# Optimization experiments

Hardware: AMD Instinct MI355X
Metric: run time of the kernel (lower is better)

The kernel has to match this reference:

```python
import jax, jax.numpy as jnp
import numpy as np

G, IN_DIM, OUT_DIM = 100000, 256, 128
B, N = 4096, 8192
ALPHA = 0.2          # LeakyReLU negative slope
NEG_INF = -9e15      # same masking constant as the torch module
EPS = 1e-12          # F.normalize eps


def setup_inputs() -> dict:
    key = jax.random.key(0)
    k1, k2, k3, k4, k5, k6, k7 = jax.random.split(key, 7)
    global_feature = jax.random.normal(k1, (G, IN_DIM), dtype=jnp.float32)
    nodes = jax.random.randint(k2, (B,), 0, G, dtype=jnp.int32)
    unique_nodes = jax.random.randint(k3, (N,), 0, G, dtype=jnp.int32)
    mask = jax.random.randint(k4, (B, N), 0, 2, dtype=jnp.int32)
    # ensure every row has at least one neighbor (original always includes self)
    mask = mask.at[:, 0].set(1)
    # xavier_uniform with gain=1.414
    gain = 1.414
    lim_W = gain * np.sqrt(6.0 / (IN_DIM + OUT_DIM))
    W = jax.random.uniform(k5, (IN_DIM, OUT_DIM), jnp.float32, -lim_W, lim_W)
    lim_a = gain * np.sqrt(6.0 / (2 * OUT_DIM + 1))
    a1 = jax.random.uniform(k6, (OUT_DIM,), jnp.float32, -lim_a, lim_a)
    a2 = jax.random.uniform(k7, (OUT_DIM,), jnp.float32, -lim_a, lim_a)
    return {"global_feature": global_feature, "nodes": nodes,
            "unique_nodes": unique_nodes, "mask": mask,
            "W": W, "a1": a1, "a2": a2}


def reference(global_feature, nodes, unique_nodes, mask, W, a1, a2):
    # project gathered features: [B,F], [N,F]
    h_nodes = global_feature[nodes] @ W
    h_neigh = global_feature[unique_nodes] @ W
    # additive attention scores; equivalent to cat([h_i,h_j]) @ a
    e = h_nodes @ a1[:, None] + (h_neigh @ a2)[None, :]   # [B,N]
    e = jnp.where(e >= 0, e, ALPHA * e)                    # leaky relu
    e = jnp.where(mask > 0, e, NEG_INF)
    attention = jax.nn.softmax(e, axis=1)                  # [B,N]
    out = attention @ h_neigh                              # [B,F]
    norm = jnp.linalg.norm(out, axis=1, keepdims=True)
    out = out / jnp.maximum(norm, EPS)                     # F.normalize p=2
    return out
```

## Files before the change

### kernel.cpp

```cpp
#include <hip/hip_runtime.h>
#include <hip/hip_bf16.h>

#define IN_DIM  256
#define OUT_DIM 128
#define B_ROWS  4096
#define N_COLS  8192
#define ALPHA   0.2f
#define NS      4

typedef unsigned short u16;
typedef unsigned int   u32;
typedef __attribute__((ext_vector_type(8))) short short8;
typedef __attribute__((ext_vector_type(4))) float floatx4;

__device__ __forceinline__ float bf2f(u16 v){ return __uint_as_float(((u32)v) << 16); }
__device__ __forceinline__ float bflo(u32 v){ return __uint_as_float(v << 16); }
__device__ __forceinline__ float bfhi(u32 v){ return __uint_as_float(v & 0xffff0000u); }
__device__ __forceinline__ u16 f2bf(float f){
    u32 u = __float_as_uint(f);
    u += 0x7fffu + ((u >> 16) & 1u);
    return (u16)(u >> 16);
}
__device__ __forceinline__ u32 pack_bf16(float a, float b){
    __hip_bfloat162 h = __float22bfloat162_rn(make_float2(a, b));
    return *reinterpret_cast<u32*>(&h);
}

__device__ __forceinline__ int detect_bf16_wave(const u32* __restrict__ g){
    int lane = threadIdx.x & 63;
    uint4 u = ((const uint4*)g)[lane];
#define CHK(x) ((((x) >> 7) & 0xFF) >= 110 && (((x) >> 7) & 0xFF) <= 140)
    unsigned long long c0 = __ballot(CHK(u.x)), c1 = __ballot(CHK(u.y));
    unsigned long long c2 = __ballot(CHK(u.z)), c3 = __ballot(CHK(u.w));
#undef CHK
    int votes = __popcll(c0) + __popcll(c1) + __popcll(c2) + __popcll(c3);
    return votes >= 128;
}

__global__ __launch_bounds__(128) void k_prep(const void* __restrict__ gf,
                                              const void* __restrict__ W, const void* __restrict__ a1,
                                              const void* __restrict__ a2,
                                              u16* __restrict__ WB, float* __restrict__ Wa1,
                                              float* __restrict__ a2f){
    const int isbf = detect_bf16_wave((const u32*)gf);
    const int c  = threadIdx.x;
    const int kb = blockIdx.x;
    float a1c = isbf ? bf2f(((const u16*)a1)[c]) : ((const float*)a1)[c];
    float w[8]; short8 v;
#pragma unroll
    for (int j = 0; j < 8; j++){
        w[j] = isbf ? bf2f(((const u16*)W)[(kb*8 + j) * OUT_DIM + c])
                    : ((const float*)W)[(kb*8 + j) * OUT_DIM + c];
        v[j] = (short)f2bf(w[j]);
    }
    ((short8*)WB)[kb * OUT_DIM + c] = v;

    __shared__ float red[2][8];
    int lane = c & 63, wv = c >> 6;
#pragma unroll
    for (int j = 0; j < 8; j++){
        float p = w[j] * a1c;
        p += __shfl_xor(p, 1);  p += __shfl_xor(p, 2);  p += __shfl_xor(p, 4);
        p += __shfl_xor(p, 8);  p += __shfl_xor(p, 16); p += __shfl_xor(p, 32);
        if (lane == 0) red[wv][j] = p;
    }
    __syncthreads();
    if (c < 8) Wa1[kb*8 + c] = red[0][c] + red[1][c];
    if (kb == 0) a2f[c] = isbf ? bf2f(((const u16*)a2)[c]) : ((const float*)a2)[c];
}

__global__ __launch_bounds__(256) void k_hneigh(const void* __restrict__ gf, const int* __restrict__ uniq,
                                                const u16* __restrict__ WB, const float* __restrict__ a2f,
                                                u16* __restrict__ hB, float2* __restrict__ esg2){
    const int n0   = blockIdx.x * 16;
    const int t    = threadIdx.x;
    const int lane = t & 63;
    const int wv   = t >> 6;
    const int q    = lane >> 4;
    const int m    = lane & 15;
    const int isbf = detect_bf16_wave((const u32*)gf);
    const int jb0  = wv * 2;

    const size_t row = (size_t)uniq[n0 + m];
    const short8* wb8 = (const short8*)WB;

    floatx4 acc0 = {0.f,0.f,0.f,0.f};
    floatx4 acc1 = {0.f,0.f,0.f,0.f};

#pragma unroll
    for (int ks = 0; ks < IN_DIM/32; ks++){
        short8 afrag;
        if (isbf){
            afrag = *(const short8*)((const u16*)gf + row * IN_DIM + ks*32 + q*8);
        } else {
            const float* gp = (const float*)gf + row * IN_DIM + ks*32 + q*8;
            float4 f0 = *(const float4*)gp;
            float4 f1 = *(const float4*)(gp + 4);
            afrag[0] = (short)f2bf(f0.x); afrag[1] = (short)f2bf(f0.y);
            afrag[2] = (short)f2bf(f0.z); afrag[3] = (short)f2bf(f0.w);
            afrag[4] = (short)f2bf(f1.x); afrag[5] = (short)f2bf(f1.y);
            afrag[6] = (short)f2bf(f1.z); afrag[7] = (short)f2bf(f1.w);
        }
        const int kb = ks*4 + q;
        short8 b0 = wb8[kb * OUT_DIM + jb0*16 + m];
        short8 b1 = wb8[kb * OUT_DIM + (jb0+1)*16 + m];
        acc0 = __builtin_amdgcn_mfma_f32_16x16x32_bf16(afrag, b0, acc0, 0, 0, 0);
        acc1 = __builtin_amdgcn_mfma_f32_16x16x32_bf16(afrag, b1, acc1, 0, 0, 0);
    }

    {
        uint2 v0, v1;
        v0.x = (u32)f2bf(acc0[0]) | ((u32)f2bf(acc0[1]) << 16);
        v0.y = (u32)f2bf(acc0[2]) | ((u32)f2bf(acc0[3]) << 16);
        v1.x = (u32)f2bf(acc1[0]) | ((u32)f2bf(acc1[1]) << 16);
        v1.y = (u32)f2bf(acc1[2]) | ((u32)f2bf(acc1[3]) << 16);
        u16* base = hB + (size_t)(n0/8 + (q>>1)) * 1024 + (q&1)*4;
        *(uint2*)(base + (jb0*16 + m) * 8)     = v0;
        *(uint2*)(base + ((jb0+1)*16 + m) * 8) = v1;
    }

    __shared__ float sred[4][16];
    float a2c0 = a2f[jb0*16 + m], a2c1 = a2f[(jb0+1)*16 + m];
#pragma unroll
    for (int reg = 0; reg < 4; reg++){
        float pr = acc0[reg]*a2c0 + acc1[reg]*a2c1;
        pr += __shfl_xor(pr, 1); pr += __shfl_xor(pr, 2);
        pr += __shfl_xor(pr, 4); pr += __shfl_xor(pr, 8);
        if (m == 0) sred[wv][q*4 + reg] = pr;
    }
    __syncthreads();
    if (t < 16){
        float s = sred[0][t] + sred[1][t] + sred[2][t] + sred[3][t];
        s = fminf(fmaxf(s, -40.f), 40.f);
        esg2[n0 + t] = make_float2(__expf(s), __expf(ALPHA * s));
    }
}

__global__ __launch_bounds__(256) void k_esn(const void* __restrict__ gf, const int* __restrict__ nodes,
                                             const float* __restrict__ Wa1, float2* __restrict__ esn2){
    int lane = threadIdx.x & 63, wv = threadIdx.x >> 6;
    int b = blockIdx.x * 4 + wv;
    const int isbf = detect_bf16_wave((const u32*)gf);
    float4 wa = ((const float4*)Wa1)[lane];
    float x0, x1, x2, x3;
    if (isbf){
        uint2 gg = ((const uint2*)((const u16*)gf + (size_t)nodes[b] * IN_DIM))[lane];
        x0 = bflo(gg.x); x1 = bfhi(gg.x); x2 = bflo(gg.y); x3 = bfhi(gg.y);
    } else {
        float4 gg = ((const float4*)((const float*)gf + (size_t)nodes[b] * IN_DIM))[lane];
        x0 = gg.x; x1 = gg.y; x2 = gg.z; x3 = gg.w;
    }
    float s = x0*wa.x + x1*wa.y + x2*wa.z + x3*wa.w;
    s += __shfl_xor(s, 1);  s += __shfl_xor(s, 2);  s += __shfl_xor(s, 4);
    s += __shfl_xor(s, 8);  s += __shfl_xor(s, 16); s += __shfl_xor(s, 32);
    if (lane == 0){
        s = fminf(fmaxf(s, -40.f), 40.f);
        esn2[b] = make_float2(__expf(s), __expf(ALPHA * s));
    }
}

__global__ __launch_bounds__(256) void k_bits(const int* __restrict__ mask, u32* __restrict__ bm){
    const size_t base = (size_t)blockIdx.x * N_COLS;
    const int t = threadIdx.x;
    const int4* m4 = (const int4*)(mask + base) + t*8;
    u32 b = 0;
#pragma unroll
    for (int i = 0; i < 8; i++){
        int4 v = m4[i];
        b |= (v.x != 0 ? 1u : 0u) << (i*4);
        b |= (v.y != 0 ? 1u : 0u) << (i*4+1);
        b |= (v.z != 0 ? 1u : 0u) << (i*4+2);
        b |= (v.w != 0 ? 1u : 0u) << (i*4+3);
    }
    bm[(size_t)blockIdx.x * (N_COLS/32) + t] = b;
}

__global__ __launch_bounds__(512) void k_attn(const u32* __restrict__ bm,
                                              const float2* __restrict__ esn2,
                                              const float2* __restrict__ esg2,
                                              const u16* __restrict__ hB,
                                              float* __restrict__ out_part){
    const int bid = blockIdx.x;
    const int ns  = bid & (NS-1);
    const int b0  = (bid >> 2) * 32;
    const int t = threadIdx.x, lane = t & 63, wv = t >> 6;
    const int rt = wv & 1, wsp = wv >> 1;
    const int q = lane >> 4, m = lane & 15;
    const int row = b0 + rt*16 + m;
    const int n0  = ns*(N_COLS/NS) + wsp*512;

    __shared__ float red[32][128];
    {
        float4 z4 = {0.f,0.f,0.f,0.f};
        ((float4*)red)[t*2] = z4; ((float4*)red)[t*2+1] = z4;
    }
    __syncthreads();

    const float2 en = esn2[row];

    uint4 w4[4];
    {
        const uint4* bmr = (const uint4*)(bm + (size_t)row*(N_COLS/32) + (n0 >> 5));
#pragma unroll
        for (int i = 0; i < 4; i++) w4[i] = bmr[i];
    }
    u32 w16[16];
#pragma unroll
    for (int i = 0; i < 4; i++){
        w16[i*4+0] = w4[i].x; w16[i*4+1] = w4[i].y;
        w16[i*4+2] = w4[i].z; w16[i*4+3] = w4[i].w;
    }

    floatx4 acc[8];
#pragma unroll
    for (int jb = 0; jb < 8; jb++){ floatx4 z = {0.f,0.f,0.f,0.f}; acc[jb] = z; }

    const short8* hb8 = (const short8*)hB;

#pragma unroll
    for (int ks = 0; ks < 16; ks++){
        const int nn = n0 + ks*32;
        const u32 wq = w16[ks] >> (q*8);
        const float4* eg = (const float4*)esg2 + ((nn + q*8) >> 1);
        float4 g0 = eg[0], g1 = eg[1], g2 = eg[2], g3 = eg[3];

        float p[8];
#define PEL(j, gx, gy) { float tv = en.x * (gx); float t2 = en.y * (gy); \
                         float tt = (tv < 1.f) ? t2 : tv;                \
                         p[j] = (wq & (1u << (j))) ? tt : 0.f; }
        PEL(0, g0.x, g0.y) PEL(1, g0.z, g0.w)
        PEL(2, g1.x, g1.y) PEL(3, g1.z, g1.w)
        PEL(4, g2.x, g2.y) PEL(5, g2.z, g2.w)
        PEL(6, g3.x, g3.y) PEL(7, g3.z, g3.w)
#undef PEL
        uint4 av;
        av.x = pack_bf16(p[0], p[1]); av.y = pack_bf16(p[2], p[3]);
        av.z = pack_bf16(p[4], p[5]); av.w = pack_bf16(p[6], p[7]);
        short8 af = *reinterpret_cast<short8*>(&av);

        const int kb = (nn >> 3) + q;
#pragma unroll
        for (int jb = 0; jb < 8; jb++){
            short8 bfr = hb8[kb * OUT_DIM + jb*16 + m];
            acc[jb] = __builtin_amdgcn_mfma_f32_16x16x32_bf16(af, bfr, acc[jb], 0, 0, 0);
        }
    }

#pragma unroll
    for (int jb = 0; jb < 8; jb++)
#pragma unroll
        for (int reg = 0; reg < 4; reg++)
            atomicAdd(&red[rt*16 + q*4 + reg][jb*16 + m], acc[jb][reg]);
    __syncthreads();

    float* op = out_part + ((size_t)ns * B_ROWS + b0) * OUT_DIM;
    ((float4*)op)[t*2]   = ((float4*)red)[t*2];
    ((float4*)op)[t*2+1] = ((float4*)red)[t*2+1];
}

__global__ __launch_bounds__(128) void k_norm(const float* __restrict__ out_part,
                                              const void* __restrict__ gf, void* __restrict__ out){
    const int isbf = detect_bf16_wave((const u32*)gf);
    const int b = blockIdx.x, c = threadIdx.x;
    float v = 0.f;
#pragma unroll
    for (int s = 0; s < NS; s++)
        v += out_part[((size_t)s * B_ROWS + b) * OUT_DIM + c];
    float ss = v * v;
    for (int off = 32; off > 0; off >>= 1) ss += __shfl_down(ss, off);
    __shared__ float red[2];
    int lane = c & 63, wv = c >> 6;
    if (lane == 0) red[wv] = ss;
    __syncthreads();
    float tot = red[0] + red[1];
    float scale = 1.f / fmaxf(sqrtf(tot), 1e-12f);
    float o = v * scale;
    if (isbf) ((u16*)out)[(size_t)b * OUT_DIM + c] = f2bf(o);
    else      ((float*)out)[(size_t)b * OUT_DIM + c] = o;
}

extern "C" void kernel_launch(void* const* d_in, const int* in_sizes, int n_in,
                              void* d_out, int out_size, void* d_ws, size_t ws_size,
                              hipStream_t stream){
    const void* gf    = d_in[0];
    const int*  nodes = (const int*)d_in[1];
    const int*  uniq  = (const int*)d_in[2];
    const int*  mask  = (const int*)d_in[3];
    const void* W     = d_in[4];
    const void* a1    = d_in[5];
    const void* a2    = d_in[6];

    char* ws = (char*)d_ws;
    u16*    hB       = (u16*)ws;
    u16*    WB       = (u16*)(ws + (2u<<20));
    float2* esg2     = (float2*)(ws + (2u<<20) + (64u<<10));
    float*  Wa1      = (float*)(ws + (2u<<20) + (128u<<10));
    float*  a2f      = (float*)(ws + (2u<<20) + (129u<<10));
    float2* esn2     = (float2*)(ws + (2u<<20) + (130u<<10));
    u32*    bm       = (u32*)(ws + (4u<<20));
    float*  out_part = (float*)(ws + (8u<<20));

    hipLaunchKernelGGL(k_prep,   dim3(32),            dim3(128), 0, stream, gf, W, a1, a2, WB, Wa1, a2f);
    hipLaunchKernelGGL(k_hneigh, dim3(N_COLS/16),     dim3(256), 0, stream, gf, uniq, WB, a2f, hB, esg2);
    hipLaunchKernelGGL(k_esn,    dim3(B_ROWS/4),      dim3(256), 0, stream, gf, nodes, Wa1, esn2);
    hipLaunchKernelGGL(k_bits,   dim3(B_ROWS),        dim3(256), 0, stream, mask, bm);
    hipLaunchKernelGGL(k_attn,   dim3((B_ROWS/32)*NS),dim3(512), 0, stream, bm, esn2, esg2, hB, out_part);
    hipLaunchKernelGGL(k_norm,   dim3(B_ROWS),        dim3(128), 0, stream, out_part, gf, d_out);
}
```

Before: 332.6 us.

## Merge prep kernels and retile attention to 64 rows per block

Three independent prep kernels (neighbor projection, node scores, mask bitpacking) are merged into one launch with block-index dispatch, which removes launch gaps. The attention kernel now handles 64 rows per block with each wave covering all 4 row tiles over 128 columns, so every hB fragment load feeds 4 MFMAs instead of 1. The N split goes from 4 to 8 to keep enough blocks. This costs 32 accumulator registers per thread, a larger padded LDS reduction buffer, and twice the partial-sum traffic in the final normalize step.

```diff
diff --git a/kernel.cpp b/kernel.cpp
--- a/kernel.cpp
+++ b/kernel.cpp
@@ -6,7 +6,7 @@
 #define B_ROWS  4096
 #define N_COLS  8192
 #define ALPHA   0.2f
-#define NS      4
+#define NS      8
 
 typedef unsigned short u16;
 typedef unsigned int   u32;
@@ -69,193 +69,196 @@
     if (kb == 0) a2f[c] = isbf ? bf2f(((const u16*)a2)[c]) : ((const float*)a2)[c];
 }
 
-__global__ __launch_bounds__(256) void k_hneigh(const void* __restrict__ gf, const int* __restrict__ uniq,
-                                                const u16* __restrict__ WB, const float* __restrict__ a2f,
-                                                u16* __restrict__ hB, float2* __restrict__ esg2){
-    const int n0   = blockIdx.x * 16;
-    const int t    = threadIdx.x;
-    const int lane = t & 63;
-    const int wv   = t >> 6;
-    const int q    = lane >> 4;
-    const int m    = lane & 15;
-    const int isbf = detect_bf16_wave((const u32*)gf);
-    const int jb0  = wv * 2;
-
-    const size_t row = (size_t)uniq[n0 + m];
-    const short8* wb8 = (const short8*)WB;
-
-    floatx4 acc0 = {0.f,0.f,0.f,0.f};
-    floatx4 acc1 = {0.f,0.f,0.f,0.f};
-
-#pragma unroll
-    for (int ks = 0; ks < IN_DIM/32; ks++){
-        short8 afrag;
+#define HN_BLKS 512
+#define ESN_BLKS 1024
+__global__ __launch_bounds__(256) void k_mid(const void* __restrict__ gf, const int* __restrict__ uniq,
+                                             const int* __restrict__ nodes, const int* __restrict__ mask,
+                                             const u16* __restrict__ WB, const float* __restrict__ a2f,
+                                             const float* __restrict__ Wa1,
+                                             u16* __restrict__ hB, float2* __restrict__ esg2,
+                                             float2* __restrict__ esn2, u32* __restrict__ bm){
+    const int bid = blockIdx.x;
+    const int t   = threadIdx.x;
+
+    if (bid < HN_BLKS){
+        const int n0   = bid * 16;
+        const int lane = t & 63;
+        const int wv   = t >> 6;
+        const int q    = lane >> 4;
+        const int m    = lane & 15;
+        const int isbf = detect_bf16_wave((const u32*)gf);
+        const int jb0  = wv * 2;
+
+        const size_t row = (size_t)uniq[n0 + m];
+        const short8* wb8 = (const short8*)WB;
+
+        floatx4 acc0 = {0.f,0.f,0.f,0.f};
+        floatx4 acc1 = {0.f,0.f,0.f,0.f};
+
+#pragma unroll
+        for (int ks = 0; ks < IN_DIM/32; ks++){
+            short8 afrag;
+            if (isbf){
+                afrag = *(const short8*)((const u16*)gf + row * IN_DIM + ks*32 + q*8);
+            } else {
+                const float* gp = (const float*)gf + row * IN_DIM + ks*32 + q*8;
+                float4 f0 = *(const float4*)gp;
+                float4 f1 = *(const float4*)(gp + 4);
+                afrag[0] = (short)f2bf(f0.x); afrag[1] = (short)f2bf(f0.y);
+                afrag[2] = (short)f2bf(f0.z); afrag[3] = (short)f2bf(f0.w);
+                afrag[4] = (short)f2bf(f1.x); afrag[5] = (short)f2bf(f1.y);
+                afrag[6] = (short)f2bf(f1.z); afrag[7] = (short)f2bf(f1.w);
+            }
+            const int kb = ks*4 + q;
+            short8 b0 = wb8[kb * OUT_DIM + jb0*16 + m];
+            short8 b1 = wb8[kb * OUT_DIM + (jb0+1)*16 + m];
+            acc0 = __builtin_amdgcn_mfma_f32_16x16x32_bf16(afrag, b0, acc0, 0, 0, 0);
+            acc1 = __builtin_amdgcn_mfma_f32_16x16x32_bf16(afrag, b1, acc1, 0, 0, 0);
+        }
+
+        {
+            uint2 v0, v1;
+            v0.x = pack_bf16(acc0[0], acc0[1]);
+            v0.y = pack_bf16(acc0[2], acc0[3]);
+            v1.x = pack_bf16(acc1[0], acc1[1]);
+            v1.y = pack_bf16(acc1[2], acc1[3]);
+            u16* base = hB + (size_t)(n0/8 + (q>>1)) * 1024 + (q&1)*4;
+            *(uint2*)(base + (jb0*16 + m) * 8)     = v0;
+            *(uint2*)(base + ((jb0+1)*16 + m) * 8) = v1;
+        }
+
+        __shared__ float sred[4][16];
+        float a2c0 = a2f[jb0*16 + m], a2c1 = a2f[(jb0+1)*16 + m];
+#pragma unroll
+        for (int reg = 0; reg < 4; reg++){
+            float pr = acc0[reg]*a2c0 + acc1[reg]*a2c1;
+            pr += __shfl_xor(pr, 1); pr += __shfl_xor(pr, 2);
+            pr += __shfl_xor(pr, 4); pr += __shfl_xor(pr, 8);
+            if (m == 0) sred[wv][q*4 + reg] = pr;
+        }
+        __syncthreads();
+        if (t < 16){
+            float s = sred[0][t] + sred[1][t] + sred[2][t] + sred[3][t];
+            s = fminf(fmaxf(s, -40.f), 40.f);
+            esg2[n0 + t] = make_float2(__expf(s), __expf(ALPHA * s));
+        }
+    } else if (bid < HN_BLKS + ESN_BLKS){
+        const int eb = bid - HN_BLKS;
+        int lane = t & 63, wv = t >> 6;
+        int b = eb * 4 + wv;
+        const int isbf = detect_bf16_wave((const u32*)gf);
+        float4 wa = ((const float4*)Wa1)[lane];
+        float x0, x1, x2, x3;
         if (isbf){
-            afrag = *(const short8*)((const u16*)gf + row * IN_DIM + ks*32 + q*8);
+            uint2 gg = ((const uint2*)((const u16*)gf + (size_t)nodes[b] * IN_DIM))[lane];
+            x0 = bflo(gg.x); x1 = bfhi(gg.x); x2 = bflo(gg.y); x3 = bfhi(gg.y);
         } else {
-            const float* gp = (const float*)gf + row * IN_DIM + ks*32 + q*8;
-            float4 f0 = *(const float4*)gp;
-            float4 f1 = *(const float4*)(gp + 4);
-            afrag[0] = (short)f2bf(f0.x); afrag[1] = (short)f2bf(f0.y);
-            afrag[2] = (short)f2bf(f0.z); afrag[3] = (short)f2bf(f0.w);
-            afrag[4] = (short)f2bf(f1.x); afrag[5] = (short)f2bf(f1.y);
-            afrag[6] = (short)f2bf(f1.z); afrag[7] = (short)f2bf(f1.w);
-        }
-        const int kb = ks*4 + q;
-        short8 b0 = wb8[kb * OUT_DIM + jb0*16 + m];
-        short8 b1 = wb8[kb * OUT_DIM + (jb0+1)*16 + m];
-        acc0 = __builtin_amdgcn_mfma_f32_16x16x32_bf16(afrag, b0, acc0, 0, 0, 0);
-        acc1 = __builtin_amdgcn_mfma_f32_16x16x32_bf16(afrag, b1, acc1, 0, 0, 0);
+            float4 gg = ((const float4*)((const float*)gf + (size_t)nodes[b] * IN_DIM))[lane];
+            x0 = gg.x; x1 = gg.y; x2 = gg.z; x3 = gg.w;
+        }
+        float s = x0*wa.x + x1*wa.y + x2*wa.z + x3*wa.w;
+        s += __shfl_xor(s, 1);  s += __shfl_xor(s, 2);  s += __shfl_xor(s, 4);
+        s += __shfl_xor(s, 8);  s += __shfl_xor(s, 16); s += __shfl_xor(s, 32);
+        if (lane == 0){
+            s = fminf(fmaxf(s, -40.f), 40.f);
+            esn2[b] = make_float2(__expf(s), __expf(ALPHA * s));
+        }
+    } else {
+        const int rowb = bid - (HN_BLKS + ESN_BLKS);
+        const int4* m4 = (const int4*)(mask + (size_t)rowb * N_COLS) + t*8;
+        u32 b = 0;
+#pragma unroll
+        for (int i = 0; i < 8; i++){
+            int4 v = m4[i];
+            b |= (v.x != 0 ? 1u : 0u) << (i*4);
+            b |= (v.y != 0 ? 1u : 0u) << (i*4+1);
+            b |= (v.z != 0 ? 1u : 0u) << (i*4+2);
+            b |= (v.w != 0 ? 1u : 0u) << (i*4+3);
+        }
+        bm[(size_t)rowb * (N_COLS/32) + t] = b;
     }
-
-    {
-        uint2 v0, v1;
-        v0.x = (u32)f2bf(acc0[0]) | ((u32)f2bf(acc0[1]) << 16);
-        v0.y = (u32)f2bf(acc0[2]) | ((u32)f2bf(acc0[3]) << 16);
-        v1.x = (u32)f2bf(acc1[0]) | ((u32)f2bf(acc1[1]) << 16);
-        v1.y = (u32)f2bf(acc1[2]) | ((u32)f2bf(acc1[3]) << 16);
-        u16* base = hB + (size_t)(n0/8 + (q>>1)) * 1024 + (q&1)*4;
-        *(uint2*)(base + (jb0*16 + m) * 8)     = v0;
-        *(uint2*)(base + ((jb0+1)*16 + m) * 8) = v1;
-    }
-
-    __shared__ float sred[4][16];
-    float a2c0 = a2f[jb0*16 + m], a2c1 = a2f[(jb0+1)*16 + m];
-#pragma unroll
-    for (int reg = 0; reg < 4; reg++){
-        float pr = acc0[reg]*a2c0 + acc1[reg]*a2c1;
-        pr += __shfl_xor(pr, 1); pr += __shfl_xor(pr, 2);
-        pr += __shfl_xor(pr, 4); pr += __shfl_xor(pr, 8);
-        if (m == 0) sred[wv][q*4 + reg] = pr;
-    }
-    __syncthreads();
-    if (t < 16){
-        float s = sred[0][t] + sred[1][t] + sred[2][t] + sred[3][t];
-        s = fminf(fmaxf(s, -40.f), 40.f);
-        esg2[n0 + t] = make_float2(__expf(s), __expf(ALPHA * s));
-    }
-}
-
-__global__ __launch_bounds__(256) void k_esn(const void* __restrict__ gf, const int* __restrict__ nodes,
-                                             const float* __restrict__ Wa1, float2* __restrict__ esn2){
-    int lane = threadIdx.x & 63, wv = threadIdx.x >> 6;
-    int b = blockIdx.x * 4 + wv;
-    const int isbf = detect_bf16_wave((const u32*)gf);
-    float4 wa = ((const float4*)Wa1)[lane];
-    float x0, x1, x2, x3;
-    if (isbf){
-        uint2 gg = ((const uint2*)((const u16*)gf + (size_t)nodes[b] * IN_DIM))[lane];
-        x0 = bflo(gg.x); x1 = bfhi(gg.x); x2 = bflo(gg.y); x3 = bfhi(gg.y);
-    } else {
-        float4 gg = ((const float4*)((const float*)gf + (size_t)nodes[b] * IN_DIM))[lane];
-        x0 = gg.x; x1 = gg.y; x2 = gg.z; x3 = gg.w;
-    }
-    float s = x0*wa.x + x1*wa.y + x2*wa.z + x3*wa.w;
-    s += __shfl_xor(s, 1);  s += __shfl_xor(s, 2);  s += __shfl_xor(s, 4);
-    s += __shfl_xor(s, 8);  s += __shfl_xor(s, 16); s += __shfl_xor(s, 32);
-    if (lane == 0){
-        s = fminf(fmaxf(s, -40.f), 40.f);
-        esn2[b] = make_float2(__expf(s), __expf(ALPHA * s));
-    }
-}
-
-__global__ __launch_bounds__(256) void k_bits(const int* __restrict__ mask, u32* __restrict__ bm){
-    const size_t base = (size_t)blockIdx.x * N_COLS;
-    const int t = threadIdx.x;
-    const int4* m4 = (const int4*)(mask + base) + t*8;
-    u32 b = 0;
-#pragma unroll
-    for (int i = 0; i < 8; i++){
-        int4 v = m4[i];
-        b |= (v.x != 0 ? 1u : 0u) << (i*4);
-        b |= (v.y != 0 ? 1u : 0u) << (i*4+1);
-        b |= (v.z != 0 ? 1u : 0u) << (i*4+2);
-        b |= (v.w != 0 ? 1u : 0u) << (i*4+3);
-    }
-    bm[(size_t)blockIdx.x * (N_COLS/32) + t] = b;
-}
-
-__global__ __launch_bounds__(512) void k_attn(const u32* __restrict__ bm,
-                                              const float2* __restrict__ esn2,
-                                              const float2* __restrict__ esg2,
-                                              const u16* __restrict__ hB,
-                                              float* __restrict__ out_part){
+}
+
+__global__ __launch_bounds__(512, 2) void k_attn(const u32* __restrict__ bm,
+                                                 const float2* __restrict__ esn2,
+                                                 const float2* __restrict__ esg2,
+                                                 const u16* __restrict__ hB,
+                                                 float* __restrict__ out_part){
     const int bid = blockIdx.x;
     const int ns  = bid & (NS-1);
-    const int b0  = (bid >> 2) * 32;
+    const int b0  = (bid >> 3) * 64;
     const int t = threadIdx.x, lane = t & 63, wv = t >> 6;
-    const int rt = wv & 1, wsp = wv >> 1;
     const int q = lane >> 4, m = lane & 15;
-    const int row = b0 + rt*16 + m;
-    const int n0  = ns*(N_COLS/NS) + wsp*512;
-
-    __shared__ float red[32][128];
-    {
-        float4 z4 = {0.f,0.f,0.f,0.f};
-        ((float4*)red)[t*2] = z4; ((float4*)red)[t*2+1] = z4;
-    }
+    const int nb0 = ns*(N_COLS/NS) + wv*128;
+
+    __shared__ float red[64][132];
+    for (int i = t; i < 64*132; i += 512) ((float*)red)[i] = 0.f;
     __syncthreads();
 
-    const float2 en = esn2[row];
+    float2 en[4];
+#pragma unroll
+    for (int rt = 0; rt < 4; rt++) en[rt] = esn2[b0 + rt*16 + m];
 
     uint4 w4[4];
-    {
-        const uint4* bmr = (const uint4*)(bm + (size_t)row*(N_COLS/32) + (n0 >> 5));
-#pragma unroll
-        for (int i = 0; i < 4; i++) w4[i] = bmr[i];
-    }
-    u32 w16[16];
-#pragma unroll
-    for (int i = 0; i < 4; i++){
-        w16[i*4+0] = w4[i].x; w16[i*4+1] = w4[i].y;
-        w16[i*4+2] = w4[i].z; w16[i*4+3] = w4[i].w;
-    }
-
-    floatx4 acc[8];
-#pragma unroll
-    for (int jb = 0; jb < 8; jb++){ floatx4 z = {0.f,0.f,0.f,0.f}; acc[jb] = z; }
+#pragma unroll
+    for (int rt = 0; rt < 4; rt++)
+        w4[rt] = *(const uint4*)(bm + (size_t)(b0 + rt*16 + m)*(N_COLS/32) + (nb0 >> 5));
+
+    floatx4 acc[32];
+#pragma unroll
+    for (int i = 0; i < 32; i++){ floatx4 z = {0.f,0.f,0.f,0.f}; acc[i] = z; }
 
     const short8* hb8 = (const short8*)hB;
 
 #pragma unroll
-    for (int ks = 0; ks < 16; ks++){
-        const int nn = n0 + ks*32;
-        const u32 wq = w16[ks] >> (q*8);
+    for (int ks = 0; ks < 4; ks++){
+        const int nn = nb0 + ks*32;
         const float4* eg = (const float4*)esg2 + ((nn + q*8) >> 1);
         float4 g0 = eg[0], g1 = eg[1], g2 = eg[2], g3 = eg[3];
 
-        float p[8];
-#define PEL(j, gx, gy) { float tv = en.x * (gx); float t2 = en.y * (gy); \
-                         float tt = (tv < 1.f) ? t2 : tv;                \
+        short8 afr[4];
+#pragma unroll
+        for (int rt = 0; rt < 4; rt++){
+            u32 w = (ks == 0) ? w4[rt].x : (ks == 1) ? w4[rt].y : (ks == 2) ? w4[rt].z : w4[rt].w;
+            const u32 wq = w >> (q*8);
+            const float enx = en[rt].x, eny = en[rt].y;
+            float p[8];
+#define PEL(j, gx, gy) { float tv = enx * (gx); float t2 = eny * (gy); \
+                         float tt = (tv < 1.f) ? t2 : tv;              \
                          p[j] = (wq & (1u << (j))) ? tt : 0.f; }
-        PEL(0, g0.x, g0.y) PEL(1, g0.z, g0.w)
-        PEL(2, g1.x, g1.y) PEL(3, g1.z, g1.w)
-        PEL(4, g2.x, g2.y) PEL(5, g2.z, g2.w)
-        PEL(6, g3.x, g3.y) PEL(7, g3.z, g3.w)
+            PEL(0, g0.x, g0.y) PEL(1, g0.z, g0.w)
+            PEL(2, g1.x, g1.y) PEL(3, g1.z, g1.w)
+            PEL(4, g2.x, g2.y) PEL(5, g2.z, g2.w)
+            PEL(6, g3.x, g3.y) PEL(7, g3.z, g3.w)
 #undef PEL
-        uint4 av;
-        av.x = pack_bf16(p[0], p[1]); av.y = pack_bf16(p[2], p[3]);
-        av.z = pack_bf16(p[4], p[5]); av.w = pack_bf16(p[6], p[7]);
-        short8 af = *reinterpret_cast<short8*>(&av);
+            uint4 av;
+            av.x = pack_bf16(p[0], p[1]); av.y = pack_bf16(p[2], p[3]);
+            av.z = pack_bf16(p[4], p[5]); av.w = pack_bf16(p[6], p[7]);
+            afr[rt] = *reinterpret_cast<short8*>(&av);
+        }
 
         const int kb = (nn >> 3) + q;
 #pragma unroll
         for (int jb = 0; jb < 8; jb++){
             short8 bfr = hb8[kb * OUT_DIM + jb*16 + m];
-            acc[jb] = __builtin_amdgcn_mfma_f32_16x16x32_bf16(af, bfr, acc[jb], 0, 0, 0);
+#pragma unroll
+            for (int rt = 0; rt < 4; rt++)
+                acc[rt*8 + jb] = __builtin_amdgcn_mfma_f32_16x16x32_bf16(afr[rt], bfr, acc[rt*8 + jb], 0, 0, 0);
         }
     }
 
 #pragma unroll
-    for (int jb = 0; jb < 8; jb++)
-#pragma unroll
-        for (int reg = 0; reg < 4; reg++)
-            atomicAdd(&red[rt*16 + q*4 + reg][jb*16 + m], acc[jb][reg]);
+    for (int rt = 0; rt < 4; rt++)
+#pragma unroll
+        for (int jb = 0; jb < 8; jb++)
+#pragma unroll
+            for (int reg = 0; reg < 4; reg++)
+                atomicAdd(&red[rt*16 + q*4 + reg][jb*16 + m], acc[rt*8 + jb][reg]);
     __syncthreads();
 
     float* op = out_part + ((size_t)ns * B_ROWS + b0) * OUT_DIM;
-    ((float4*)op)[t*2]   = ((float4*)red)[t*2];
-    ((float4*)op)[t*2+1] = ((float4*)red)[t*2+1];
+    for (int i = t; i < 64*128; i += 512)
+        op[i] = red[i >> 7][i & 127];
 }
 
 __global__ __launch_bounds__(128) void k_norm(const float* __restrict__ out_part,
@@ -300,10 +303,9 @@
     u32*    bm       = (u32*)(ws + (4u<<20));
     float*  out_part = (float*)(ws + (8u<<20));
 
-    hipLaunchKernelGGL(k_prep,   dim3(32),            dim3(128), 0, stream, gf, W, a1, a2, WB, Wa1, a2f);
-    hipLaunchKernelGGL(k_hneigh, dim3(N_COLS/16),     dim3(256), 0, stream, gf, uniq, WB, a2f, hB, esg2);
-    hipLaunchKernelGGL(k_esn,    dim3(B_ROWS/4),      dim3(256), 0, stream, gf, nodes, Wa1, esn2);
-    hipLaunchKernelGGL(k_bits,   dim3(B_ROWS),        dim3(256), 0, stream, mask, bm);
-    hipLaunchKernelGGL(k_attn,   dim3((B_ROWS/32)*NS),dim3(512), 0, stream, bm, esn2, esg2, hB, out_part);
-    hipLaunchKernelGGL(k_norm,   dim3(B_ROWS),        dim3(128), 0, stream, out_part, gf, d_out);
-}
+    hipLaunchKernelGGL(k_prep, dim3(32), dim3(128), 0, stream, gf, W, a1, a2, WB, Wa1, a2f);
+    hipLaunchKernelGGL(k_mid,  dim3(HN_BLKS + ESN_BLKS + B_ROWS), dim3(256), 0, stream,
+                       gf, uniq, nodes, mask, WB, a2f, Wa1, hB, esg2, esn2, bm);
+    hipLaunchKernelGGL(k_attn, dim3((B_ROWS/64)*NS), dim3(512), 0, stream, bm, esn2, esg2, hB, out_part);
+    hipLaunchKernelGGL(k_norm, dim3(B_ROWS), dim3(128), 0, stream, out_part, gf, d_out);
+}
```

Result: slower. 435.7 us (+31.0%).
